# Kernel tuning notes

Measured on AMD Instinct MI355X. Metric: run time of the kernel, lower is better.

## Reference

```python
import jax, jax.numpy as jnp
import numpy as np

M_BIT = 8      # BfpConfig.bfp_M_Bit (sign + mantissa bits)
BLOCK = 64     # BFP block size along contraction (K) dim
K_SIZE, STRIDE, PAD = 3, 1, 1


def bfp_quantize(x, m_bit=M_BIT, block=BLOCK):
    """Block-floating-point quantize along last axis: per-block shared exponent
    from max-abs, m_bit-wide signed mantissa, then dequantize back to fp."""
    shape = x.shape
    xb = x.reshape(shape[:-1] + (shape[-1] // block, block))
    maxabs = jnp.max(jnp.abs(xb), axis=-1, keepdims=True)
    exp = jnp.floor(jnp.log2(jnp.maximum(maxabs, jnp.float32(1e-38))))
    scale = jnp.exp2(exp - (m_bit - 2))          # lsb weight for this block
    qmax = jnp.float32(2.0 ** (m_bit - 1) - 1)
    q = jnp.clip(jnp.round(xb / scale), -qmax - 1.0, qmax) * scale
    q = jnp.where(maxabs == 0.0, 0.0, q)
    return q.reshape(shape)


def im2col(x, k, s, p):
    """Torch Unfold ordering: columns flattened as (C, kh, kw). x: [N,C,H,W]."""
    N, C, H, W = x.shape
    Ho = (H + 2 * p - k) // s + 1
    Wo = (W + 2 * p - k) // s + 1
    xp = jnp.pad(x, ((0, 0), (0, 0), (p, p), (p, p)))
    rows = []
    for i in range(k):
        for j in range(k):
            rows.append(xp[:, :, i:i + s * Ho:s, j:j + s * Wo:s])  # [N,C,Ho,Wo]
    # [k*k, N, C, Ho, Wo] -> [N, C, k*k, Ho*Wo] -> [N, C*k*k, Ho*Wo]
    patches = jnp.stack(rows, axis=0).transpose(1, 2, 0, 3, 4)
    return patches.reshape(N, C * k * k, Ho * Wo), Ho, Wo


def setup_inputs() -> dict:
    key = jax.random.key(0)
    k1, k2, k3 = jax.random.split(key, 3)
    inputs = jax.random.normal(k1, (32, 128, 56, 56), dtype=jnp.float32)
    fan_in = 128 * K_SIZE * K_SIZE
    weight = jax.random.normal(k2, (256, 128, K_SIZE, K_SIZE), dtype=jnp.float32) / np.sqrt(fan_in)
    bias = jax.random.normal(k3, (256,), dtype=jnp.float32) * 0.01
    return {"inputs": inputs, "weight": weight, "bias": bias}


def reference(inputs, weight, bias):
    N = inputs.shape[0]
    C_out = weight.shape[0]
    cols, Ho, Wo = im2col(inputs, K_SIZE, STRIDE, PAD)      # [N, K, Ho*Wo]
    a = cols.transpose(0, 2, 1).reshape(-1, cols.shape[1])  # [N*Ho*Wo, K]
    w = weight.reshape(C_out, -1)                           # [C_out, K]
    qa = bfp_quantize(a)
    qw = bfp_quantize(w)
    out = qa @ qw.T + bias                                  # [N*Ho*Wo, C_out]
    out = out.reshape(N, Ho, Wo, C_out).transpose(0, 3, 1, 2)
    return out
```

## Files before the change

kernel.cpp:

```cpp
#include <hip/hip_runtime.h>

typedef short short8 __attribute__((ext_vector_type(8)));
typedef __bf16 bf16x8 __attribute__((ext_vector_type(8)));
typedef float floatx4 __attribute__((ext_vector_type(4)));

__device__ __forceinline__ float make_pow2(int e) {
  return __builtin_bit_cast(float, (unsigned)((e + 127) << 23));
}

typedef __attribute__((address_space(3))) void lds_void;
typedef const __attribute__((address_space(1))) void glob_void;
__device__ __forceinline__ void gload_lds16(const void* g, void* l) {
  __builtin_amdgcn_global_load_lds((glob_void*)g, (lds_void*)l, 16, 0, 0);
}

__global__ void quant_w_kernel(const float* __restrict__ w, unsigned short* __restrict__ qw) {
  int b = blockIdx.x;
  int row = b / 18, kb = b - row * 18;
  int t = threadIdx.x;
  int idx = row * 1152 + kb * 64 + t;
  float v = w[idx];
  float a = fabsf(v);
  #pragma unroll
  for (int off = 32; off; off >>= 1) a = fmaxf(a, __shfl_xor(a, off));
  float q = 0.f;
  if (a > 0.f) {
    int e = (int)((__builtin_bit_cast(unsigned, a) >> 23) & 0xffu) - 127;
    if (e < -126) e = -126;
    float inv = make_pow2(6 - e);
    float s   = make_pow2(e - 6);
    float r = rintf(v * inv);
    r = fminf(fmaxf(r, -128.f), 127.f);
    q = r * s;
  }
  qw[idx] = (unsigned short)(__builtin_bit_cast(unsigned, q) >> 16);
}

__global__ __launch_bounds__(256) void conv_bfp_kernel(
    const float* __restrict__ in, const unsigned short* __restrict__ qw,
    const float* __restrict__ bias, float* __restrict__ out) {
  __shared__ unsigned short As[64 * 64];
  __shared__ unsigned short Bs[256 * 64];
  __shared__ float pmax[64][4];

  const int mt = blockIdx.x;
  const int t = threadIdx.x;
  const int lane = t & 63;
  const int wave = __builtin_amdgcn_readfirstlane(t >> 6);

  const unsigned m = mt * 64u + lane;
  const unsigned nimg = m / 3136u;
  const unsigned py = m - nimg * 3136u;
  const int y = (int)(py / 56u);
  const int x = (int)(py - (unsigned)y * 56u);
  const int vbase = (int)((nimg * 401408u + (unsigned)y * 56u + (unsigned)x) * 4u);
  int vm = 0;
  #pragma unroll
  for (int i = 0; i < 3; ++i)
    #pragma unroll
    for (int j = 0; j < 3; ++j)
      if ((unsigned)(y + i - 1) < 56u && (unsigned)(x + j - 1) < 56u)
        vm |= 1 << (i * 3 + j);

  const int l3 = lane >> 3, l7 = lane & 7;
  const char* bsrc = (const char*)qw + (size_t)((wave * 64 + l3) * 2304) + ((l7 ^ l3) * 16);
  char* bdst = (char*)Bs + wave * 8192;

  const int lr = lane & 15;
  const int lk = (lane >> 4) << 4;
  const int swz = (lr & 7) << 4;

  floatx4 acc[4][4] = {};

  for (int kb = 0; kb < 18; ++kb) {
    float av[16];
    float lmax = 0.f;
    const int k0 = __builtin_amdgcn_readfirstlane(kb * 64 + wave * 16);
    #pragma unroll
    for (int u = 0; u < 16; ++u) {
      int k = k0 + u;
      int c = (int)((unsigned)k / 9u);
      int ij = k - c * 9;
      int soff = c * 3136 + (ij / 3) * 56 + (ij % 3) - 57;
      const char* pk = (const char*)in + (ptrdiff_t)soff * 4;
      float v = 0.f;
      if ((vm >> ij) & 1)
        v = *(const float*)(pk + vbase);
      av[u] = v;
      lmax = fmaxf(lmax, fabsf(v));
    }
    pmax[lane][wave] = lmax;
    __syncthreads();

    #pragma unroll
    for (int c8 = 0; c8 < 8; ++c8)
      gload_lds16(bsrc + (size_t)c8 * 18432 + kb * 128, bdst + c8 * 1024);

    floatx4 pm = *(floatx4*)&pmax[lane][0];
    float ma = fmaxf(fmaxf(pm[0], pm[1]), fmaxf(pm[2], pm[3]));
    short8 aq0, aq1;
    if (ma > 0.f) {
      int e = (int)((__builtin_bit_cast(unsigned, ma) >> 23) & 0xffu) - 127;
      if (e < -126) e = -126;
      float inv = make_pow2(6 - e);
      float s   = make_pow2(e - 6);
      #pragma unroll
      for (int u = 0; u < 16; ++u) {
        float r = rintf(av[u] * inv);
        r = fminf(fmaxf(r, -128.f), 127.f);
        float q = r * s;
        unsigned short hb = (unsigned short)(__builtin_bit_cast(unsigned, q) >> 16);
        if (u < 8) aq0[u] = (short)hb; else aq1[u - 8] = (short)hb;
      }
    } else {
      aq0 = (short8)0; aq1 = (short8)0;
    }
    {
      char* arow = (char*)As + lane * 128;
      int kx = wave * 32;
      *(short8*)(arow + ((kx)      ^ ((lane & 7) << 4))) = aq0;
      *(short8*)(arow + ((kx + 16) ^ ((lane & 7) << 4))) = aq1;
    }
    __syncthreads();

    #pragma unroll
    for (int ks = 0; ks < 2; ++ks) {
      const int kbyte = (ks * 64 + lk) ^ swz;
      bf16x8 afr[4], bfr[4];
      #pragma unroll
      for (int f = 0; f < 4; ++f) {
        afr[f] = __builtin_bit_cast(bf16x8,
            *(const short8*)((const char*)As + (f * 16 + lr) * 128 + kbyte));
        bfr[f] = __builtin_bit_cast(bf16x8,
            *(const short8*)((const char*)Bs + (wave * 64 + f * 16 + lr) * 128 + kbyte));
      }
      #pragma unroll
      for (int fm = 0; fm < 4; ++fm)
        #pragma unroll
        for (int fn = 0; fn < 4; ++fn)
          acc[fm][fn] = __builtin_amdgcn_mfma_f32_16x16x32_bf16(afr[fm], bfr[fn], acc[fm][fn], 0, 0, 0);
    }
    if (kb < 17) __syncthreads();
  }

  const int rg = (lane >> 4) << 2;
  #pragma unroll
  for (int fm = 0; fm < 4; ++fm) {
    unsigned ni4[4], pp4[4];
    #pragma unroll
    for (int r = 0; r < 4; ++r) {
      unsigned mm = mt * 64u + fm * 16 + rg + r;
      ni4[r] = mm / 3136u;
      pp4[r] = mm - ni4[r] * 3136u;
    }
    #pragma unroll
    for (int fn = 0; fn < 4; ++fn) {
      int co = wave * 64 + fn * 16 + lr;
      float bco = bias[co];
      #pragma unroll
      for (int r = 0; r < 4; ++r)
        out[(size_t)ni4[r] * 802816u + (size_t)co * 3136u + pp4[r]] = acc[fm][fn][r] + bco;
    }
  }
}

extern "C" void kernel_launch(void* const* d_in, const int* in_sizes, int n_in,
                              void* d_out, int out_size, void* d_ws, size_t ws_size,
                              hipStream_t stream) {
  const float* in   = (const float*)d_in[0];
  const float* w    = (const float*)d_in[1];
  const float* bias = (const float*)d_in[2];
  float* out = (float*)d_out;
  unsigned short* qw = (unsigned short*)d_ws;

  quant_w_kernel<<<4608, 64, 0, stream>>>(w, qw);
  conv_bfp_kernel<<<1568, 256, 0, stream>>>(in, qw, bias, out);
}
```

Measured before the change: 151.7 us.

## Prefetch next K-block gather during MFMA and coalesce output stores via transposed accumulators

Splits the K loop into gather and step phases so the next block's input gather is issued right after the A tile is written, overlapping global-load latency with the MFMA loop. The pmax reduction buffer is double-buffered, letting the trailing barrier per iteration be removed. MFMA operands are swapped so each lane holds outputs along the spatial dimension, turning the NCHW epilogue into contiguous 16-wide row stores with a hoisted image index. It costs extra registers for a second 16-float prefetch buffer, which may reduce occupancy.

```diff
diff --git a/kernel.cpp b/kernel.cpp
--- a/kernel.cpp
+++ b/kernel.cpp
@@ -41,7 +41,7 @@
     const float* __restrict__ bias, float* __restrict__ out) {
   __shared__ unsigned short As[64 * 64];
   __shared__ unsigned short Bs[256 * 64];
-  __shared__ float pmax[64][4];
+  __shared__ float pmax[2][64][4];
 
   const int mt = blockIdx.x;
   const int t = threadIdx.x;
@@ -72,9 +72,7 @@
 
   floatx4 acc[4][4] = {};
 
-  for (int kb = 0; kb < 18; ++kb) {
-    float av[16];
-    float lmax = 0.f;
+  auto gather = [&](float (&av)[16], int kb) {
     const int k0 = __builtin_amdgcn_readfirstlane(kb * 64 + wave * 16);
     #pragma unroll
     for (int u = 0; u < 16; ++u) {
@@ -87,16 +85,21 @@
       if ((vm >> ij) & 1)
         v = *(const float*)(pk + vbase);
       av[u] = v;
-      lmax = fmaxf(lmax, fabsf(v));
     }
-    pmax[lane][wave] = lmax;
+  };
+
+  auto step = [&](float (&avc)[16], float (&avn)[16], int kb) {
+    float lmax = 0.f;
+    #pragma unroll
+    for (int u = 0; u < 16; ++u) lmax = fmaxf(lmax, fabsf(avc[u]));
+    pmax[kb & 1][lane][wave] = lmax;
     __syncthreads();
 
     #pragma unroll
     for (int c8 = 0; c8 < 8; ++c8)
       gload_lds16(bsrc + (size_t)c8 * 18432 + kb * 128, bdst + c8 * 1024);
 
-    floatx4 pm = *(floatx4*)&pmax[lane][0];
+    floatx4 pm = *(floatx4*)&pmax[kb & 1][lane][0];
     float ma = fmaxf(fmaxf(pm[0], pm[1]), fmaxf(pm[2], pm[3]));
     short8 aq0, aq1;
     if (ma > 0.f) {
@@ -106,7 +109,7 @@
       float s   = make_pow2(e - 6);
       #pragma unroll
       for (int u = 0; u < 16; ++u) {
-        float r = rintf(av[u] * inv);
+        float r = rintf(avc[u] * inv);
         r = fminf(fmaxf(r, -128.f), 127.f);
         float q = r * s;
         unsigned short hb = (unsigned short)(__builtin_bit_cast(unsigned, q) >> 16);
@@ -123,6 +126,8 @@
     }
     __syncthreads();
 
+    if (kb < 17) gather(avn, kb + 1);
+
     #pragma unroll
     for (int ks = 0; ks < 2; ++ks) {
       const int kbyte = (ks * 64 + lk) ^ swz;
@@ -138,28 +143,32 @@
       for (int fm = 0; fm < 4; ++fm)
         #pragma unroll
         for (int fn = 0; fn < 4; ++fn)
-          acc[fm][fn] = __builtin_amdgcn_mfma_f32_16x16x32_bf16(afr[fm], bfr[fn], acc[fm][fn], 0, 0, 0);
+          acc[fm][fn] = __builtin_amdgcn_mfma_f32_16x16x32_bf16(bfr[fn], afr[fm], acc[fm][fn], 0, 0, 0);
     }
-    if (kb < 17) __syncthreads();
+  };
+
+  float av0[16], av1[16];
+  gather(av0, 0);
+  #pragma unroll 1
+  for (int kb = 0; kb < 18; kb += 2) {
+    step(av0, av1, kb);
+    step(av1, av0, kb + 1);
   }
 
-  const int rg = (lane >> 4) << 2;
+  const unsigned ni = (mt * 64u) / 3136u;
+  const unsigned pp0 = mt * 64u - ni * 3136u;
+  float* obase = out + (size_t)ni * 802816u + pp0;
+  const int cg = (lane >> 4) << 2;
   #pragma unroll
-  for (int fm = 0; fm < 4; ++fm) {
-    unsigned ni4[4], pp4[4];
+  for (int fn = 0; fn < 4; ++fn) {
     #pragma unroll
     for (int r = 0; r < 4; ++r) {
-      unsigned mm = mt * 64u + fm * 16 + rg + r;
-      ni4[r] = mm / 3136u;
-      pp4[r] = mm - ni4[r] * 3136u;
-    }
-    #pragma unroll
-    for (int fn = 0; fn < 4; ++fn) {
-      int co = wave * 64 + fn * 16 + lr;
+      int co = wave * 64 + fn * 16 + cg + r;
       float bco = bias[co];
+      float* orow = obase + (size_t)co * 3136u;
       #pragma unroll
-      for (int r = 0; r < 4; ++r)
-        out[(size_t)ni4[r] * 802816u + (size_t)co * 3136u + pp4[r]] = acc[fm][fn][r] + bco;
+      for (int fm = 0; fm < 4; ++fm)
+        orow[fm * 16 + lr] = acc[fm][fn][r] + bco;
     }
   }
 }
```

New measurement: 166.0 us. 1.09x slower.
